# Performance work log

Measured on AMD Instinct MI355X. Metric: run time of the kernel, lower is better.

The kernel has to match this reference:

```python
import jax, jax.numpy as jnp
import numpy as np

N, E = 50000, 800000
INDIM, HID, OUT = 128, 256, 47
DENSITY = 0.5
EPS = 1e-5


def _masked_glorot(key, fan_in, fan_out):
    kw, km = jax.random.split(key)
    lim = np.sqrt(6.0 / (fan_in + fan_out))
    w = jax.random.uniform(kw, (fan_in, fan_out), jnp.float32, -lim, lim)
    mask = (jax.random.uniform(km, (fan_in, fan_out)) < DENSITY).astype(jnp.float32)
    return w * mask  # expander sparsity pre-applied to the weight


def setup_inputs() -> dict:
    key = jax.random.key(0)
    ks = jax.random.split(key, 12)
    x = jax.random.normal(ks[0], (N, INDIM), jnp.float32)
    edge_index = jax.random.randint(ks[1], (2, E), 0, N, jnp.int64)
    d = {
        "x": x,
        "edge_index": edge_index,
        "w1l": _masked_glorot(ks[2], INDIM, HID),
        "w1r": _masked_glorot(ks[3], INDIM, HID),
        "b1": jnp.zeros((HID,), jnp.float32),
        "g1": jnp.ones((HID,), jnp.float32),
        "be1": jnp.zeros((HID,), jnp.float32),
        "w2l": _masked_glorot(ks[4], HID, HID),
        "w2r": _masked_glorot(ks[5], HID, HID),
        "b2": jnp.zeros((HID,), jnp.float32),
        "g2": jnp.ones((HID,), jnp.float32),
        "be2": jnp.zeros((HID,), jnp.float32),
        "w3l": _masked_glorot(ks[6], HID, OUT),
        "w3r": _masked_glorot(ks[7], HID, OUT),
        "b3": jnp.zeros((OUT,), jnp.float32),
    }
    return d


def reference(x, edge_index, w1l, w1r, b1, g1, be1, w2l, w2r, b2, g2, be2, w3l, w3r, b3):
    src, dst = edge_index[0], edge_index[1]
    n = x.shape[0]
    deg = jax.ops.segment_sum(jnp.ones(src.shape[0], x.dtype), dst, num_segments=n)
    inv_deg = 1.0 / jnp.maximum(deg, 1.0)  # [N]

    def sage(h, wl, wr, b):
        # mean-aggregate neighbor features (gather + segment_sum), then masked linears
        agg = jax.ops.segment_sum(h[src], dst, num_segments=n) * inv_deg[:, None]
        return agg @ wl + h @ wr + b

    def bn(h, g, b):
        mu = h.mean(axis=0)
        var = h.var(axis=0)
        return g * (h - mu) * jax.lax.rsqrt(var + EPS) + b

    h = jax.nn.relu(bn(sage(x, w1l, w1r, b1), g1, be1))
    h = jax.nn.relu(bn(sage(h, w2l, w2r, b2), g2, be2))
    h = sage(h, w3l, w3r, b3)
    return jax.nn.log_softmax(h, axis=-1)
```

## Files before the change

kernel.cpp:

```cpp
#include <hip/hip_runtime.h>
#include <hip/hip_bf16.h>
#include <cmath>

#define EPS 1e-5f

typedef __attribute__((ext_vector_type(8))) short bf16x8;
typedef __attribute__((ext_vector_type(4))) float f32x4;
typedef __attribute__((ext_vector_type(2))) float floatx2;

static __device__ __forceinline__ ushort f32_to_bf16(float f) {
    __hip_bfloat16 h = __float2bfloat16(f);
    return __builtin_bit_cast(ushort, h);
}
static __device__ __forceinline__ float blo(unsigned u) { return __uint_as_float(u << 16); }
static __device__ __forceinline__ float bhi(unsigned u) { return __uint_as_float(u & 0xffff0000u); }
static __device__ __forceinline__ unsigned bpack(float a, float b) {
    return (unsigned)f32_to_bf16(a) | ((unsigned)f32_to_bf16(b) << 16);
}
static __device__ __forceinline__ unsigned char f32_to_fp8(float v) {
    return (unsigned char)(__builtin_amdgcn_cvt_pk_fp8_f32(v, 0.f, 0, false) & 0xff);
}

static __device__ __forceinline__ void async16(const void* g, void* l) {
    __builtin_amdgcn_global_load_lds(
        (const __attribute__((address_space(1))) unsigned int*)g,
        (__attribute__((address_space(3))) unsigned int*)l, 16, 0, 0);
}

#define DEC8(u) { floatx2 p_; \
    p_ = __builtin_amdgcn_cvt_pk_f32_fp8((int)(u).x, false); a0 += p_.x; a1 += p_.y; \
    p_ = __builtin_amdgcn_cvt_pk_f32_fp8((int)(u).x, true);  a2 += p_.x; a3 += p_.y; \
    p_ = __builtin_amdgcn_cvt_pk_f32_fp8((int)(u).y, false); a4 += p_.x; a5 += p_.y; \
    p_ = __builtin_amdgcn_cvt_pk_f32_fp8((int)(u).y, true);  a6 += p_.x; a7 += p_.y; }
#define DEC4(u) { floatx2 p_; \
    p_ = __builtin_amdgcn_cvt_pk_f32_fp8((int)(u), false); a0 += p_.x; a1 += p_.y; \
    p_ = __builtin_amdgcn_cvt_pk_f32_fp8((int)(u), true);  a2 += p_.x; a3 += p_.y; }


__global__ void k_pre(const int* __restrict__ dst, int E, int* __restrict__ gcnt,
                      const float* __restrict__ x, ushort* __restrict__ cat1,
                      unsigned char* __restrict__ xq, int NX,
                      const float* __restrict__ w1l, const float* __restrict__ w1r,
                      const float* __restrict__ w2l, const float* __restrict__ w2r,
                      const float* __restrict__ w3l, const float* __restrict__ w3r,
                      ushort* __restrict__ Wt1, ushort* __restrict__ Wt2,
                      ushort* __restrict__ Wt3, int bktB, int cvtB) {
    int b = blockIdx.x;
    int t = threadIdx.x;
    if (b < bktB) {
        __shared__ int hist[256];
        hist[t] = 0;
        __syncthreads();
        int base = b * 8192;
        int end = base + 8192; if (end > E) end = E;
        for (int i = base + t; i < end; i += 256)
            atomicAdd(&hist[((unsigned)dst[i]) >> 8], 1);
        __syncthreads();
        if (hist[t]) atomicAdd(&gcnt[t], hist[t]);
    } else if (b < bktB + cvtB) {
        int i = (b - bktB) * 256 + t;
        if (i < NX) {
            int row = i >> 7, c = i & 127;
            float v = x[i];
            cat1[(size_t)row * 256 + 128 + c] = f32_to_bf16(v);
            xq[(size_t)row * 128 + c] = f32_to_fp8(v);
        }
    } else {
        int tt = (b - bktB - cvtB) * 256 + t;
        if (tt < 128 * 256) {
            int k = tt >> 8, c = tt & 255;
            Wt1[(size_t)c * 256 + k] = f32_to_bf16(w1l[tt]);
            Wt1[(size_t)c * 256 + 128 + k] = f32_to_bf16(w1r[tt]);
        }
        if (tt < 256 * 256) {
            int k = tt >> 8, c = tt & 255;
            Wt2[(size_t)c * 512 + k] = f32_to_bf16(w2l[tt]);
            Wt2[(size_t)c * 512 + 256 + k] = f32_to_bf16(w2r[tt]);
        }
        if (tt < 256 * 47) {
            int k = tt / 47, c = tt - k * 47;
            Wt3[(size_t)c * 256 + k] = f32_to_bf16(w3l[tt]);
            Wt3[(size_t)(64 + c) * 256 + k] = f32_to_bf16(w3r[tt]);
        }
    }
}

__global__ void k_bscan(const int* __restrict__ gcnt, int* __restrict__ gbase,
                        int* __restrict__ gtail, int NB) {
    __shared__ int s[256];
    int t = threadIdx.x;
    int v = (t < NB) ? gcnt[t] : 0;
    s[t] = v;
    __syncthreads();
    for (int off = 1; off < 256; off <<= 1) {
        int add = (t >= off) ? s[t - off] : 0;
        __syncthreads();
        s[t] += add;
        __syncthreads();
    }
    int excl = s[t] - v;
    if (t < NB) { gbase[t] = excl; gtail[t] = excl; }
}

__global__ void k_scatter(const int* __restrict__ src, const int* __restrict__ dst,
                          int E, int* __restrict__ gtail, uint2* __restrict__ pairs,
                          int NB) {
    __shared__ int hist[256];
    __shared__ int lcur[256];
    int t = threadIdx.x;
    hist[t] = 0;
    __syncthreads();
    int base = blockIdx.x * 8192;
    int end = base + 8192; if (end > E) end = E;
    for (int i = base + t; i < end; i += 256)
        atomicAdd(&hist[((unsigned)dst[i]) >> 8], 1);
    __syncthreads();
    if (t < NB && hist[t]) lcur[t] = atomicAdd(&gtail[t], hist[t]);
    __syncthreads();
    for (int i = base + t; i < end; i += 256) {
        int dd = dst[i];
        int pos = atomicAdd(&lcur[((unsigned)dd) >> 8], 1);
        pairs[pos] = make_uint2((unsigned)src[i], (unsigned)dd);
    }
}

__global__ void k_brow(const uint2* __restrict__ pairs, const int* __restrict__ gbase,
                       const int* __restrict__ gcnt, int* __restrict__ row_ptr,
                       float* __restrict__ inv_deg, int N, int E) {
    int b = blockIdx.x;
    __shared__ int hist[256];
    __shared__ int sc[256];
    int t = threadIdx.x;
    hist[t] = 0;
    __syncthreads();
    int s = gbase[b], cnt = gcnt[b];
    for (int i = t; i < cnt; i += 256) {
        uint2 p = pairs[s + i];
        atomicAdd(&hist[p.y & 255], 1);
    }
    __syncthreads();
    int d = hist[t];
    sc[t] = d;
    __syncthreads();
    for (int off = 1; off < 256; off <<= 1) {
        int add = (t >= off) ? sc[t - off] : 0;
        __syncthreads();
        sc[t] += add;
        __syncthreads();
    }
    int node = b * 256 + t;
    if (node < N) {
        row_ptr[node] = s + sc[t] - d;
        inv_deg[node] = 1.0f / (float)(d > 1 ? d : 1);
    }
    if (b == 0 && t == 0) row_ptr[N] = E;
}

__global__ void k_bfill(const uint2* __restrict__ pairs, const int* __restrict__ gbase,
                        const int* __restrict__ gcnt, const int* __restrict__ row_ptr,
                        int* __restrict__ colidx, int N) {
    int b = blockIdx.x;
    __shared__ int cur[256];
    int t = threadIdx.x;
    int node = b * 256 + t;
    cur[t] = (node < N) ? row_ptr[node] : 0;
    __syncthreads();
    int s = gbase[b], cnt = gcnt[b];
    for (int i = t; i < cnt; i += 256) {
        uint2 p = pairs[s + i];
        int pos = atomicAdd(&cur[p.y & 255], 1);
        colidx[pos] = (int)p.x;
    }
}


__global__ void k_agg256q(const unsigned char* __restrict__ hq, const int* __restrict__ rp,
                          const int* __restrict__ ci, const float* __restrict__ inv_deg,
                          ushort* __restrict__ out, int ldo, int N) {
    int wid = (blockIdx.x * blockDim.x + threadIdx.x) >> 6;
    int lane = threadIdx.x & 63;
    if (wid >= N) return;
    int s = rp[wid], e = rp[wid + 1];
    int half = lane >> 5, l32 = lane & 31;
    int cnt = e - s;
    int n_my = (cnt - half + 1) >> 1;
    int i = s + half;
    float a0 = 0, a1 = 0, a2 = 0, a3 = 0, a4 = 0, a5 = 0, a6 = 0, a7 = 0;
    size_t lo = (size_t)l32 * 8;
    while (n_my >= 4) {
        int c0 = ci[i], c1 = ci[i + 2], c2 = ci[i + 4], c3 = ci[i + 6];
        uint2 u0 = *reinterpret_cast<const uint2*>(hq + (size_t)c0 * 256 + lo);
        uint2 u1 = *reinterpret_cast<const uint2*>(hq + (size_t)c1 * 256 + lo);
        uint2 u2 = *reinterpret_cast<const uint2*>(hq + (size_t)c2 * 256 + lo);
        uint2 u3 = *reinterpret_cast<const uint2*>(hq + (size_t)c3 * 256 + lo);
        DEC8(u0); DEC8(u1); DEC8(u2); DEC8(u3);
        i += 8; n_my -= 4;
    }
    while (n_my > 0) {
        int c = ci[i];
        uint2 u = *reinterpret_cast<const uint2*>(hq + (size_t)c * 256 + lo);
        DEC8(u);
        i += 2; n_my--;
    }
    a0 += __shfl_xor(a0, 32, 64); a1 += __shfl_xor(a1, 32, 64);
    a2 += __shfl_xor(a2, 32, 64); a3 += __shfl_xor(a3, 32, 64);
    a4 += __shfl_xor(a4, 32, 64); a5 += __shfl_xor(a5, 32, 64);
    a6 += __shfl_xor(a6, 32, 64); a7 += __shfl_xor(a7, 32, 64);
    if (half == 0) {
        float id = inv_deg[wid];
        uint4 o;
        o.x = bpack(a0 * id, a1 * id); o.y = bpack(a2 * id, a3 * id);
        o.z = bpack(a4 * id, a5 * id); o.w = bpack(a6 * id, a7 * id);
        *reinterpret_cast<uint4*>(out + (size_t)wid * ldo + l32 * 8) = o;
    }
}

__global__ void k_agg128q(const unsigned char* __restrict__ hq, const int* __restrict__ rp,
                          const int* __restrict__ ci, const float* __restrict__ inv_deg,
                          ushort* __restrict__ out, int ldo, int N) {
    int wid = (blockIdx.x * blockDim.x + threadIdx.x) >> 6;
    int lane = threadIdx.x & 63;
    if (wid >= N) return;
    int s = rp[wid], e = rp[wid + 1];
    int g = lane >> 4, l16 = lane & 15;
    int cnt = e - s;
    int n_my = (cnt - g + 3) >> 2;
    int i = s + g;
    float a0 = 0, a1 = 0, a2 = 0, a3 = 0, a4 = 0, a5 = 0, a6 = 0, a7 = 0;
    size_t lo = (size_t)l16 * 8;
    while (n_my >= 4) {
        int c0 = ci[i], c1 = ci[i + 4], c2 = ci[i + 8], c3 = ci[i + 12];
        uint2 u0 = *reinterpret_cast<const uint2*>(hq + (size_t)c0 * 128 + lo);
        uint2 u1 = *reinterpret_cast<const uint2*>(hq + (size_t)c1 * 128 + lo);
        uint2 u2 = *reinterpret_cast<const uint2*>(hq + (size_t)c2 * 128 + lo);
        uint2 u3 = *reinterpret_cast<const uint2*>(hq + (size_t)c3 * 128 + lo);
        DEC8(u0); DEC8(u1); DEC8(u2); DEC8(u3);
        i += 16; n_my -= 4;
    }
    while (n_my > 0) {
        int c = ci[i];
        uint2 u = *reinterpret_cast<const uint2*>(hq + (size_t)c * 128 + lo);
        DEC8(u);
        i += 4; n_my--;
    }
#pragma unroll
    for (int off = 16; off <= 32; off <<= 1) {
        a0 += __shfl_xor(a0, off, 64); a1 += __shfl_xor(a1, off, 64);
        a2 += __shfl_xor(a2, off, 64); a3 += __shfl_xor(a3, off, 64);
        a4 += __shfl_xor(a4, off, 64); a5 += __shfl_xor(a5, off, 64);
        a6 += __shfl_xor(a6, off, 64); a7 += __shfl_xor(a7, off, 64);
    }
    if (lane < 16) {
        float id = inv_deg[wid];
        uint4 o;
        o.x = bpack(a0 * id, a1 * id); o.y = bpack(a2 * id, a3 * id);
        o.z = bpack(a4 * id, a5 * id); o.w = bpack(a6 * id, a7 * id);
        *reinterpret_cast<uint4*>(out + (size_t)wid * ldo + l16 * 8) = o;
    }
}

__global__ void k_agg47fq(const unsigned char* __restrict__ p3q, const int* __restrict__ rp,
                          const int* __restrict__ ci, const float* __restrict__ inv_deg,
                          const float* __restrict__ q3, float* __restrict__ out,
                          int N, int OUTD) {
    int wid = (blockIdx.x * blockDim.x + threadIdx.x) >> 6;
    int lane = threadIdx.x & 63;
    if (wid >= N) return;
    int s = rp[wid], e = rp[wid + 1];
    int g = lane >> 4, l16 = lane & 15;
    int cnt = e - s;
    int n_my = (cnt - g + 3) >> 2;
    int i = s + g;
    float a0 = 0, a1 = 0, a2 = 0, a3 = 0;
    size_t lo = (size_t)l16 * 4;
    while (n_my >= 4) {
        int c0 = ci[i], c1 = ci[i + 4], c2 = ci[i + 8], c3 = ci[i + 12];
        unsigned u0 = *reinterpret_cast<const unsigned*>(p3q + (size_t)c0 * 64 + lo);
        unsigned u1 = *reinterpret_cast<const unsigned*>(p3q + (size_t)c1 * 64 + lo);
        unsigned u2 = *reinterpret_cast<const unsigned*>(p3q + (size_t)c2 * 64 + lo);
        unsigned u3 = *reinterpret_cast<const unsigned*>(p3q + (size_t)c3 * 64 + lo);
        DEC4(u0); DEC4(u1); DEC4(u2); DEC4(u3);
        i += 16; n_my -= 4;
    }
    while (n_my > 0) {
        int c = ci[i];
        unsigned u = *reinterpret_cast<const unsigned*>(p3q + (size_t)c * 64 + lo);
        DEC4(u);
        i += 4; n_my--;
    }
#pragma unroll
    for (int off = 16; off <= 32; off <<= 1) {
        a0 += __shfl_xor(a0, off, 64); a1 += __shfl_xor(a1, off, 64);
        a2 += __shfl_xor(a2, off, 64); a3 += __shfl_xor(a3, off, 64);
    }
    float id = inv_deg[wid];
    int c0 = l16 * 4;
    float z0 = (c0 + 0 < OUTD) ? a0 * id + q3[(size_t)wid * 48 + c0 + 0] : -INFINITY;
    float z1 = (c0 + 1 < OUTD) ? a1 * id + q3[(size_t)wid * 48 + c0 + 1] : -INFINITY;
    float z2 = (c0 + 2 < OUTD) ? a2 * id + q3[(size_t)wid * 48 + c0 + 2] : -INFINITY;
    float z3 = (c0 + 3 < OUTD) ? a3 * id + q3[(size_t)wid * 48 + c0 + 3] : -INFINITY;
    float m = fmaxf(fmaxf(z0, z1), fmaxf(z2, z3));
#pragma unroll
    for (int off = 1; off <= 8; off <<= 1) m = fmaxf(m, __shfl_xor(m, off, 64));
    float es = ((c0 + 0 < OUTD) ? __expf(z0 - m) : 0.f) + ((c0 + 1 < OUTD) ? __expf(z1 - m) : 0.f)
             + ((c0 + 2 < OUTD) ? __expf(z2 - m) : 0.f) + ((c0 + 3 < OUTD) ? __expf(z3 - m) : 0.f);
#pragma unroll
    for (int off = 1; off <= 8; off <<= 1) es += __shfl_xor(es, off, 64);
    float ls = __logf(es) + m;
    if (lane < 16) {
        if (c0 + 0 < OUTD) out[(size_t)wid * OUTD + c0 + 0] = z0 - ls;
        if (c0 + 1 < OUTD) out[(size_t)wid * OUTD + c0 + 1] = z1 - ls;
        if (c0 + 2 < OUTD) out[(size_t)wid * OUTD + c0 + 2] = z2 - ls;
        if (c0 + 3 < OUTD) out[(size_t)wid * OUTD + c0 + 3] = z3 - ls;
    }
}


template <int EPI>
__global__ __launch_bounds__(256) void k_mgemm(
    const ushort* __restrict__ A, const ushort* __restrict__ Wt,
    const float* __restrict__ bias, ushort* __restrict__ outb,
    unsigned char* __restrict__ outq,
    float* __restrict__ q3, float* __restrict__ psum, float* __restrict__ psq,
    int Nrows, int K, int M) {
    __shared__ __align__(16) ushort sA[4][64 * 32];
    __shared__ __align__(16) ushort sB[4][128 * 32];
    __shared__ float red[2][2][4][16][2];
    const int tid = threadIdx.x;
    const int w = tid >> 6, l = tid & 63;
    const int wr = w >> 1, wc = w & 1;
    const int row0 = blockIdx.x * 64, col0 = blockIdx.y * 128;
    const int li = l & 15, kg = l >> 4;

    const int rA = tid >> 2, kgpA = tid & 3;
    const int kglA = (kgpA - (rA >> 1)) & 3;
    int grA = row0 + rA; if (grA >= Nrows) grA = Nrows - 1;
    const ushort* gpA = A + (size_t)grA * K + kglA * 8;

    const int rB0 = tid >> 2, kglB0 = ((tid & 3) - (rB0 >> 1)) & 3;
    const ushort* gpB0 = Wt + (size_t)(col0 + rB0) * K + kglB0 * 8;
    const int cB1 = tid + 256;
    const int rB1 = cB1 >> 2, kglB1 = ((cB1 & 3) - (rB1 >> 1)) & 3;
    const ushort* gpB1 = Wt + (size_t)(col0 + rB1) * K + kglB1 * 8;

    const int nk = K >> 5;

    auto stageT = [&](int t) {
        const int kt = t << 5;
        const int buf = t & 3;
        async16(gpA + kt, &sA[buf][(size_t)tid * 8]);
        async16(gpB0 + kt, &sB[buf][(size_t)tid * 8]);
        async16(gpB1 + kt, &sB[buf][(size_t)cB1 * 8]);
    };

    stageT(0);
    if (nk > 1) stageT(1);
    if (nk > 2) stageT(2);

    f32x4 acc[2][4] = {};

    for (int t = 0; t < nk; ++t) {
        int rem = ((t + 3 < nk) ? t + 3 : nk) - (t + 1);
        if (rem == 2)      asm volatile("s_waitcnt vmcnt(6)" ::: "memory");
        else if (rem == 1) asm volatile("s_waitcnt vmcnt(3)" ::: "memory");
        else               asm volatile("s_waitcnt vmcnt(0)" ::: "memory");
        __builtin_amdgcn_s_barrier();
        __builtin_amdgcn_sched_barrier(0);

        if (t + 3 < nk) stageT(t + 3);

        const int buf = t & 3;
        bf16x8 af[2], bfr[4];
#pragma unroll
        for (int m = 0; m < 2; m++) {
            int r = wr * 32 + m * 16 + li;
            af[m] = *reinterpret_cast<const bf16x8*>(&sA[buf][(r * 4 + ((kg + (r >> 1)) & 3)) * 8]);
        }
#pragma unroll
        for (int n = 0; n < 4; n++) {
            int r = wc * 64 + n * 16 + li;
            bfr[n] = *reinterpret_cast<const bf16x8*>(&sB[buf][(r * 4 + ((kg + (r >> 1)) & 3)) * 8]);
        }
#pragma unroll
        for (int m = 0; m < 2; m++)
#pragma unroll
            for (int n = 0; n < 4; n++)
                acc[m][n] = __builtin_amdgcn_mfma_f32_16x16x32_bf16(af[m], bfr[n], acc[m][n], 0, 0, 0);
        __builtin_amdgcn_sched_barrier(0);
    }

    if constexpr (EPI == 2) {
#pragma unroll
        for (int n = 0; n < 4; n++) {
            int col = col0 + wc * 64 + n * 16 + li;
            float b = bias[col];
            float s = 0.f, sq = 0.f;
#pragma unroll
            for (int m = 0; m < 2; m++) {
                int rbase = row0 + wr * 32 + m * 16 + kg * 4;
#pragma unroll
                for (int qi = 0; qi < 4; qi++) {
                    int row = rbase + qi;
                    if (row < Nrows) {
                        float v = acc[m][n][qi] + b;
                        outb[(size_t)row * M + col] = f32_to_bf16(v);
                        s += v; sq += v * v;
                    }
                }
            }
            s += __shfl_xor(s, 16, 64); s += __shfl_xor(s, 32, 64);
            sq += __shfl_xor(sq, 16, 64); sq += __shfl_xor(sq, 32, 64);
            if (kg == 0) { red[wr][wc][n][li][0] = s; red[wr][wc][n][li][1] = sq; }
        }
        __syncthreads();
        if (wr == 0 && kg == 0) {
#pragma unroll
            for (int n = 0; n < 4; n++) {
                int gcol = col0 + wc * 64 + n * 16 + li;
                psum[(size_t)blockIdx.x * 256 + gcol] = red[0][wc][n][li][0] + red[1][wc][n][li][0];
                psq[(size_t)blockIdx.x * 256 + gcol] = red[0][wc][n][li][1] + red[1][wc][n][li][1];
            }
        }
    } else {
#pragma unroll
        for (int n = 0; n < 4; n++) {
            int col = wc * 64 + n * 16 + li;
#pragma unroll
            for (int m = 0; m < 2; m++) {
                int rbase = row0 + wr * 32 + m * 16 + kg * 4;
#pragma unroll
                for (int qi = 0; qi < 4; qi++) {
                    int row = rbase + qi;
                    if (row >= Nrows) continue;
                    float v = acc[m][n][qi];
                    if (wc == 0) {
                        outq[(size_t)row * 64 + col] = f32_to_fp8(col < 47 ? v : 0.f);
                    } else {
                        int qc = col - 64;
                        if (qc < 47) q3[(size_t)row * 48 + qc] = v + bias[qc];
                    }
                }
            }
        }
    }
}


__global__ void k_bn_final(const float* __restrict__ psum, const float* __restrict__ psq,
                           int nb, int N, const float* __restrict__ g,
                           const float* __restrict__ be, float* __restrict__ scale,
                           float* __restrict__ shift) {
    int c = blockIdx.x;
    int t = threadIdx.x;
    float s = 0.f, q = 0.f;
    for (int b = t; b < nb; b += 256) { s += psum[(size_t)b * 256 + c]; q += psq[(size_t)b * 256 + c]; }
#pragma unroll
    for (int off = 32; off; off >>= 1) { s += __shfl_xor(s, off, 64); q += __shfl_xor(q, off, 64); }
    __shared__ float ls[4], lq[4];
    int wv = t >> 6;
    if ((t & 63) == 0) { ls[wv] = s; lq[wv] = q; }
    __syncthreads();
    if (t == 0) {
        s = ls[0] + ls[1] + ls[2] + ls[3];
        q = lq[0] + lq[1] + lq[2] + lq[3];
        float mu = s / (float)N;
        float var = q / (float)N - mu * mu;
        float sc = g[c] * rsqrtf(var + EPS);
        scale[c] = sc;
        shift[c] = be[c] - mu * sc;
    }
}

__global__ void k_bn_apply_b(const ushort* __restrict__ zb, long total8,
                             const float* __restrict__ scale, const float* __restrict__ shift,
                             ushort* __restrict__ outb, int ldo, int off,
                             unsigned char* __restrict__ hq) {
    long i = blockIdx.x * (long)blockDim.x + threadIdx.x;
    long stride = (long)gridDim.x * blockDim.x;
    for (; i < total8; i += stride) {
        long idx = i * 8;
        int row = (int)(idx >> 8);
        int c = (int)(idx & 255);
        uint4 u = *reinterpret_cast<const uint4*>(zb + idx);
        float y0 = fmaxf(blo(u.x) * scale[c + 0] + shift[c + 0], 0.f);
        float y1 = fmaxf(bhi(u.x) * scale[c + 1] + shift[c + 1], 0.f);
        float y2 = fmaxf(blo(u.y) * scale[c + 2] + shift[c + 2], 0.f);
        float y3 = fmaxf(bhi(u.y) * scale[c + 3] + shift[c + 3], 0.f);
        float y4 = fmaxf(blo(u.z) * scale[c + 4] + shift[c + 4], 0.f);
        float y5 = fmaxf(bhi(u.z) * scale[c + 5] + shift[c + 5], 0.f);
        float y6 = fmaxf(blo(u.w) * scale[c + 6] + shift[c + 6], 0.f);
        float y7 = fmaxf(bhi(u.w) * scale[c + 7] + shift[c + 7], 0.f);
        uint4 o;
        o.x = bpack(y0, y1); o.y = bpack(y2, y3); o.z = bpack(y4, y5); o.w = bpack(y6, y7);
        *reinterpret_cast<uint4*>(outb + (size_t)row * ldo + off + c) = o;
        if (hq) {
            unsigned lo8 = 0, hi8 = 0;
            lo8 = (unsigned)__builtin_amdgcn_cvt_pk_fp8_f32(y0, y1, 0, false);
            lo8 = (unsigned)__builtin_amdgcn_cvt_pk_fp8_f32(y2, y3, (int)lo8, true);
            hi8 = (unsigned)__builtin_amdgcn_cvt_pk_fp8_f32(y4, y5, 0, false);
            hi8 = (unsigned)__builtin_amdgcn_cvt_pk_fp8_f32(y6, y7, (int)hi8, true);
            *reinterpret_cast<uint2*>(hq + (size_t)row * 256 + c) = make_uint2(lo8, hi8);
        }
    }
}


extern "C" void kernel_launch(void* const* d_in, const int* in_sizes, int n_in,
                              void* d_out, int out_size, void* d_ws, size_t ws_size,
                              hipStream_t stream) {
    const float* x   = (const float*)d_in[0];
    const int*   ei  = (const int*)d_in[1];
    const float* w1l = (const float*)d_in[2];
    const float* w1r = (const float*)d_in[3];
    const float* b1  = (const float*)d_in[4];
    const float* g1  = (const float*)d_in[5];
    const float* be1 = (const float*)d_in[6];
    const float* w2l = (const float*)d_in[7];
    const float* w2r = (const float*)d_in[8];
    const float* b2  = (const float*)d_in[9];
    const float* g2  = (const float*)d_in[10];
    const float* be2 = (const float*)d_in[11];
    const float* w3l = (const float*)d_in[12];
    const float* w3r = (const float*)d_in[13];
    const float* b3  = (const float*)d_in[14];
    float* out = (float*)d_out;

    const int INDIM = 128, HID = 256;
    int N = in_sizes[0] / INDIM;
    int E = in_sizes[1] / 2;
    int OUTD = in_sizes[14];
    const int* src = ei;
    const int* dst = ei + E;
    int NB = (N + 255) >> 8;

    size_t off = 0;
    auto carve = [&](size_t bytes) -> char* {
        char* p = (char*)d_ws + off;
        off = (off + bytes + 255) & ~(size_t)255;
        return p;
    };
    int*    row_ptr  = (int*)carve((size_t)(N + 1) * 4);
    float*  inv_deg  = (float*)carve((size_t)N * 4);
    int*    gcnt     = (int*)carve(256 * 4);
    int*    gbase    = (int*)carve(256 * 4);
    int*    gtail    = (int*)carve(256 * 4);
    uint2*  pairs    = (uint2*)carve((size_t)E * 8);
    int*    colidx   = (int*)carve((size_t)E * 4);
    float*  psum     = (float*)carve((size_t)256 * 1024 * 4);
    float*  psq      = (float*)carve((size_t)256 * 1024 * 4);
    float*  bnscale  = (float*)carve(256 * 4);
    float*  bnshift  = (float*)carve(256 * 4);
    ushort* Wt1      = (ushort*)carve((size_t)256 * 256 * 2);
    ushort* Wt2      = (ushort*)carve((size_t)256 * 512 * 2);
    ushort* Wt3      = (ushort*)carve((size_t)128 * 256 * 2);
    ushort* cat1     = (ushort*)carve((size_t)N * 256 * 2);
    unsigned char* xq  = (unsigned char*)carve((size_t)N * 128);
    unsigned char* h1q = (unsigned char*)carve((size_t)N * 256);
    ushort* cat2     = (ushort*)carve((size_t)N * 512 * 2);
    ushort* zb       = (ushort*)carve((size_t)N * HID * 2);
    unsigned char* p3q = (unsigned char*)carve((size_t)N * 64);
    float*  q3       = (float*)carve((size_t)N * 48 * 4);
    (void)ws_size; (void)n_in; (void)out_size;

    hipMemsetAsync(gcnt, 0, 256 * 4, stream);
    hipMemsetAsync(Wt3, 0, (size_t)128 * 256 * 2, stream);

    int bktB = (E + 8191) / 8192;
    int cvtB = (N * 128 + 255) / 256;
    k_pre<<<bktB + cvtB + 256, 256, 0, stream>>>(dst, E, gcnt, x, cat1, xq, N * 128,
                                                 w1l, w1r, w2l, w2r, w3l, w3r,
                                                 Wt1, Wt2, Wt3, bktB, cvtB);
    k_bscan<<<1, 256, 0, stream>>>(gcnt, gbase, gtail, NB);
    k_scatter<<<bktB, 256, 0, stream>>>(src, dst, E, gtail, pairs, NB);
    k_brow<<<NB, 256, 0, stream>>>(pairs, gbase, gcnt, row_ptr, inv_deg, N, E);
    k_bfill<<<NB, 256, 0, stream>>>(pairs, gbase, gcnt, row_ptr, colidx, N);

    int aggBlocks = (N + 3) / 4;
    int MB = (N + 63) / 64;
    long total8 = (long)N * 32;
    ushort* h2b = cat2;

    k_agg128q<<<aggBlocks, 256, 0, stream>>>(xq, row_ptr, colidx, inv_deg, cat1, 256, N);
    k_mgemm<2><<<dim3(MB, 2), 256, 0, stream>>>(cat1, Wt1, b1, zb, nullptr, nullptr,
                                                psum, psq, N, 256, 256);
    k_bn_final<<<256, 256, 0, stream>>>(psum, psq, MB, N, g1, be1, bnscale, bnshift);
    k_bn_apply_b<<<1024, 256, 0, stream>>>(zb, total8, bnscale, bnshift, cat2, 512, 256, h1q);

    k_agg256q<<<aggBlocks, 256, 0, stream>>>(h1q, row_ptr, colidx, inv_deg, cat2, 512, N);
    k_mgemm<2><<<dim3(MB, 2), 256, 0, stream>>>(cat2, Wt2, b2, zb, nullptr, nullptr,
                                                psum, psq, N, 512, 256);
    k_bn_final<<<256, 256, 0, stream>>>(psum, psq, MB, N, g2, be2, bnscale, bnshift);
    k_bn_apply_b<<<1024, 256, 0, stream>>>(zb, total8, bnscale, bnshift, h2b, 256, 0, nullptr);

    k_mgemm<1><<<dim3(MB, 1), 256, 0, stream>>>(h2b, Wt3, b3, nullptr, p3q, q3,
                                                nullptr, nullptr, N, 256, 128);
    k_agg47fq<<<aggBlocks, 256, 0, stream>>>(p3q, row_ptr, colidx, inv_deg, q3, out, N, OUTD);
}
```

Baseline: 300.3 us.

## Enlarge GEMM row tile to 128 and switch to double-buffered staging

The bf16 MFMA GEMM now computes 128x128 output tiles instead of 64x128, so each wave holds a 4x4 grid of accumulators and reuses each B fragment across twice as many rows. The four-stage async LDS pipeline becomes a two-stage double buffer, with the next tile prefetched before the wait and a second barrier at the end of each iteration. The aim is to cut redundant weight loads and block count per GEMM. In exchange there is less prefetch depth, an extra barrier per k-step, more accumulator registers, and half as many blocks to spread across the CUs.

```diff
diff --git a/kernel.cpp b/kernel.cpp
--- a/kernel.cpp
+++ b/kernel.cpp
@@ -323,19 +323,22 @@
     unsigned char* __restrict__ outq,
     float* __restrict__ q3, float* __restrict__ psum, float* __restrict__ psq,
     int Nrows, int K, int M) {
-    __shared__ __align__(16) ushort sA[4][64 * 32];
-    __shared__ __align__(16) ushort sB[4][128 * 32];
+    __shared__ __align__(16) ushort sA[2][128 * 32];
+    __shared__ __align__(16) ushort sB[2][128 * 32];
     __shared__ float red[2][2][4][16][2];
     const int tid = threadIdx.x;
     const int w = tid >> 6, l = tid & 63;
     const int wr = w >> 1, wc = w & 1;
-    const int row0 = blockIdx.x * 64, col0 = blockIdx.y * 128;
+    const int row0 = blockIdx.x * 128, col0 = blockIdx.y * 128;
     const int li = l & 15, kg = l >> 4;
 
-    const int rA = tid >> 2, kgpA = tid & 3;
-    const int kglA = (kgpA - (rA >> 1)) & 3;
-    int grA = row0 + rA; if (grA >= Nrows) grA = Nrows - 1;
-    const ushort* gpA = A + (size_t)grA * K + kglA * 8;
+    const int rA0 = tid >> 2, kglA0 = ((tid & 3) - (rA0 >> 1)) & 3;
+    int grA0 = row0 + rA0; if (grA0 >= Nrows) grA0 = Nrows - 1;
+    const ushort* gpA0 = A + (size_t)grA0 * K + kglA0 * 8;
+    const int cA1 = tid + 256;
+    const int rA1 = cA1 >> 2, kglA1 = ((cA1 & 3) - (rA1 >> 1)) & 3;
+    int grA1 = row0 + rA1; if (grA1 >= Nrows) grA1 = Nrows - 1;
+    const ushort* gpA1 = A + (size_t)grA1 * K + kglA1 * 8;
 
     const int rB0 = tid >> 2, kglB0 = ((tid & 3) - (rB0 >> 1)) & 3;
     const ushort* gpB0 = Wt + (size_t)(col0 + rB0) * K + kglB0 * 8;
@@ -344,36 +347,34 @@
     const ushort* gpB1 = Wt + (size_t)(col0 + rB1) * K + kglB1 * 8;
 
     const int nk = K >> 5;
-
     auto stageT = [&](int t) {
         const int kt = t << 5;
-        const int buf = t & 3;
-        async16(gpA + kt, &sA[buf][(size_t)tid * 8]);
+        const int buf = t & 1;
+        async16(gpA0 + kt, &sA[buf][(size_t)tid * 8]);
+        async16(gpA1 + kt, &sA[buf][(size_t)cA1 * 8]);
         async16(gpB0 + kt, &sB[buf][(size_t)tid * 8]);
         async16(gpB1 + kt, &sB[buf][(size_t)cB1 * 8]);
     };
 
     stageT(0);
-    if (nk > 1) stageT(1);
-    if (nk > 2) stageT(2);
-
-    f32x4 acc[2][4] = {};
+
+    f32x4 acc[4][4] = {};
 
     for (int t = 0; t < nk; ++t) {
-        int rem = ((t + 3 < nk) ? t + 3 : nk) - (t + 1);
-        if (rem == 2)      asm volatile("s_waitcnt vmcnt(6)" ::: "memory");
-        else if (rem == 1) asm volatile("s_waitcnt vmcnt(3)" ::: "memory");
-        else               asm volatile("s_waitcnt vmcnt(0)" ::: "memory");
+        if (t + 1 < nk) {
+            stageT(t + 1);
+            asm volatile("s_waitcnt vmcnt(4)" ::: "memory");
+        } else {
+            asm volatile("s_waitcnt vmcnt(0)" ::: "memory");
+        }
         __builtin_amdgcn_s_barrier();
         __builtin_amdgcn_sched_barrier(0);
 
-        if (t + 3 < nk) stageT(t + 3);
-
-        const int buf = t & 3;
-        bf16x8 af[2], bfr[4];
-#pragma unroll
-        for (int m = 0; m < 2; m++) {
-            int r = wr * 32 + m * 16 + li;
+        const int buf = t & 1;
+        bf16x8 af[4], bfr[4];
+#pragma unroll
+        for (int m = 0; m < 4; m++) {
+            int r = wr * 64 + m * 16 + li;
             af[m] = *reinterpret_cast<const bf16x8*>(&sA[buf][(r * 4 + ((kg + (r >> 1)) & 3)) * 8]);
         }
 #pragma unroll
@@ -382,11 +383,12 @@
             bfr[n] = *reinterpret_cast<const bf16x8*>(&sB[buf][(r * 4 + ((kg + (r >> 1)) & 3)) * 8]);
         }
 #pragma unroll
-        for (int m = 0; m < 2; m++)
+        for (int m = 0; m < 4; m++)
 #pragma unroll
             for (int n = 0; n < 4; n++)
                 acc[m][n] = __builtin_amdgcn_mfma_f32_16x16x32_bf16(af[m], bfr[n], acc[m][n], 0, 0, 0);
         __builtin_amdgcn_sched_barrier(0);
+        __builtin_amdgcn_s_barrier();
     }
 
     if constexpr (EPI == 2) {
@@ -396,8 +398,8 @@
             float b = bias[col];
             float s = 0.f, sq = 0.f;
 #pragma unroll
-            for (int m = 0; m < 2; m++) {
-                int rbase = row0 + wr * 32 + m * 16 + kg * 4;
+            for (int m = 0; m < 4; m++) {
+                int rbase = row0 + wr * 64 + m * 16 + kg * 4;
 #pragma unroll
                 for (int qi = 0; qi < 4; qi++) {
                     int row = rbase + qi;
@@ -426,8 +428,8 @@
         for (int n = 0; n < 4; n++) {
             int col = wc * 64 + n * 16 + li;
 #pragma unroll
-            for (int m = 0; m < 2; m++) {
-                int rbase = row0 + wr * 32 + m * 16 + kg * 4;
+            for (int m = 0; m < 4; m++) {
+                int rbase = row0 + wr * 64 + m * 16 + kg * 4;
 #pragma unroll
                 for (int qi = 0; qi < 4; qi++) {
                     int row = rbase + qi;
@@ -576,7 +578,7 @@
     k_bfill<<<NB, 256, 0, stream>>>(pairs, gbase, gcnt, row_ptr, colidx, N);
 
     int aggBlocks = (N + 3) / 4;
-    int MB = (N + 63) / 64;
+    int MB = (N + 127) >> 7;
     long total8 = (long)N * 32;
     ushort* h2b = cat2;
 
```

Result: no change. 296.1 us (-1.4%).
